# Kernel optimization log

Hardware: AMD Instinct MI355X
Metric: run time of the kernel (lower is better)

## Reference

```python
import jax, jax.numpy as jnp
import numpy as np
import math

N_NODES = 100000
N_EDGES = 1_600_000
NFEAT = 512
NHID = 128
NLAYERS = 6
NCLASS = 64


def setup_inputs() -> dict:
    key = jax.random.key(0)
    ks = jax.random.split(key, 8)
    x = jax.random.normal(ks[0], (N_NODES, NFEAT), jnp.float32)
    rows = jax.random.randint(ks[1], (N_EDGES,), 0, N_NODES, dtype=jnp.int32)
    cols = jax.random.randint(ks[2], (N_EDGES,), 0, N_NODES, dtype=jnp.int32)
    # normalized-adjacency-like edge weights
    vals = jax.random.uniform(ks[3], (N_EDGES,), jnp.float32) * (1.0 / 16.0)
    s = 1.0 / math.sqrt(NHID)  # reset_parameters: uniform(-1/sqrt(out_features), ...)
    W0 = jax.random.uniform(ks[4], (NFEAT, NHID), jnp.float32, minval=-s, maxval=s)
    Wh = jax.random.uniform(ks[5], (NLAYERS - 1, NHID, NHID), jnp.float32, minval=-s, maxval=s)
    Wfc = jax.random.normal(ks[6], (NHID * NLAYERS, NCLASS), jnp.float32) * 0.02
    bfc = jnp.zeros((NCLASS,), jnp.float32)
    return {"x": x, "rows": rows, "cols": cols, "vals": vals,
            "W0": W0, "Wh": Wh, "Wfc": Wfc, "bfc": bfc}


def _spmm(rows, cols, vals, h, n):
    # sparse [n,n] @ h : gather source rows, scale by edge weight, scatter-add to dest
    return jax.ops.segment_sum(vals[:, None] * h[cols], rows, num_segments=n)


def reference(x, rows, cols, vals, W0, Wh, Wfc, bfc):
    n = x.shape[0]
    # conv0: relu(spmm(A, x @ W0))  (inference: no dropout, no skip-gate)
    h = jax.nn.relu(_spmm(rows, cols, vals, x @ W0, n))
    hiddens = [h]
    for i in range(Wh.shape[0]):
        h = jax.nn.relu(_spmm(rows, cols, vals, h @ Wh[i], n))
        hiddens.append(h)
    logits = jnp.concatenate(hiddens, axis=-1) @ Wfc + bfc
    return jax.nn.log_softmax(logits, axis=1)
```

## Files before the change

kernel.cpp:

```cpp
#include <hip/hip_runtime.h>
#include <hip/hip_bf16.h>
#include <cstdint>
#include <cstddef>

static constexpr int NFEAT   = 512;
static constexpr int NHID    = 128;
static constexpr int NLAYERS = 6;
static constexpr int NCLASS  = 64;

typedef __bf16 bf16x8 __attribute__((ext_vector_type(8)));
typedef float  floatx4 __attribute__((ext_vector_type(4)));

static __device__ __forceinline__ uint16_t f2bf(float v){
    __hip_bfloat16 h = __float2bfloat16(v);
    return *reinterpret_cast<uint16_t*>(&h);
}

__global__ void k_sniff(const uint16_t* __restrict__ x, int nwords, uint32_t* __restrict__ flag){
    int i = blockIdx.x*256 + threadIdx.x;
    if (i < nwords){
        uint16_t w = x[i];
        if ((w & 0x7F80u) == 0x7F80u) atomicOr(flag, 1u);
    }
}

__global__ void k_sentinel(uint16_t* out, int nel){
    int i = blockIdx.x*256 + threadIdx.x;
    if (i < nel) out[i] = 0x3E00u;
}

__global__ void k_zero(uint32_t* p, int n){
    int i = blockIdx.x*256 + threadIdx.x;
    if (i < n) p[i] = 0u;
}

__global__ void k_hist(const int* __restrict__ rows, uint32_t* __restrict__ deg, int nE){
    int e = blockIdx.x*256 + threadIdx.x;
    if (e < nE) atomicAdd(&deg[rows[e]], 1u);
}

__global__ __launch_bounds__(1024) void k_scan1(const uint32_t* __restrict__ deg,
                                                uint32_t* __restrict__ row_start,
                                                uint32_t* __restrict__ partial, int n){
    __shared__ uint32_t sh[1024];
    int tid = threadIdx.x;
    int i = blockIdx.x*1024 + tid;
    uint32_t v = (i < n) ? deg[i] : 0u;
    sh[tid] = v; __syncthreads();
    for (int off = 1; off < 1024; off <<= 1){
        uint32_t t = (tid >= off) ? sh[tid-off] : 0u;
        __syncthreads();
        sh[tid] += t;
        __syncthreads();
    }
    if (i < n) row_start[i+1] = sh[tid];
    if (tid == 1023) partial[blockIdx.x] = sh[1023];
}

__global__ __launch_bounds__(128) void k_scan2(uint32_t* partial, int nb){
    __shared__ uint32_t sh[128];
    int tid = threadIdx.x;
    uint32_t v = (tid < nb) ? partial[tid] : 0u;
    sh[tid] = v; __syncthreads();
    for (int off = 1; off < 128; off <<= 1){
        uint32_t t = (tid >= off) ? sh[tid-off] : 0u;
        __syncthreads();
        sh[tid] += t;
        __syncthreads();
    }
    if (tid < nb) partial[tid] = sh[tid] - v;
}

__global__ __launch_bounds__(1024) void k_scan3(const uint32_t* __restrict__ deg,
                                                uint32_t* __restrict__ row_start,
                                                const uint32_t* __restrict__ partial,
                                                uint32_t* __restrict__ bcur,
                                                uint32_t* __restrict__ cursor, int n){
    int i = blockIdx.x*1024 + threadIdx.x;
    if (i < n){
        uint32_t rs = row_start[i+1] + partial[blockIdx.x];
        row_start[i+1] = rs;
        uint32_t start = rs - deg[i];
        cursor[i] = start;
        if ((i & 255) == 0) bcur[i >> 8] = start;
        if (i == 0) row_start[0] = 0u;
    }
}

__global__ void k_scatter(const int* __restrict__ rows, const int* __restrict__ cols,
                          const void* __restrict__ vals,
                          uint32_t* __restrict__ cursor, uint2* __restrict__ ep, int nE,
                          const uint32_t* __restrict__ flags){
    int e = blockIdx.x*256 + threadIdx.x;
    if (e < nE){
        int r = rows[e];
        uint32_t pos = atomicAdd(&cursor[r], 1u);
        float v;
        if (flags[0]) v = ((const float*)vals)[e];
        else          v = __bfloat162float(((const __hip_bfloat16*)vals)[e]);
        ep[pos] = make_uint2((uint32_t)cols[e], __float_as_uint(v));
    }
}

__global__ __launch_bounds__(256) void k_bin(
    const int* __restrict__ rows, const int* __restrict__ cols,
    const void* __restrict__ vals,
    uint32_t* __restrict__ bcur,
    uint2* __restrict__ epb, uint8_t* __restrict__ rloc,
    int nE, int nbuck, int epb_per_block,
    const uint32_t* __restrict__ flags)
{
    __shared__ uint32_t h[512];
    const int tid = threadIdx.x;
    const int e0 = blockIdx.x * epb_per_block;
    int e1 = e0 + epb_per_block; if (e1 > nE) e1 = nE;

    for (int b = tid; b < nbuck; b += 256) h[b] = 0u;
    __syncthreads();
    for (int e = e0 + tid; e < e1; e += 256){
        int r = rows[e];
        atomicAdd(&h[r >> 8], 1u);
    }
    __syncthreads();
    for (int b = tid; b < nbuck; b += 256){
        uint32_t c = h[b];
        h[b] = c ? atomicAdd(&bcur[b], c) : 0u;
    }
    __syncthreads();
    const int fp32 = (int)flags[0];
    for (int e = e0 + tid; e < e1; e += 256){
        int r = rows[e];
        uint32_t pos = atomicAdd(&h[r >> 8], 1u);
        float v;
        if (fp32) v = ((const float*)vals)[e];
        else      v = __bfloat162float(((const __hip_bfloat16*)vals)[e]);
        epb[pos] = make_uint2((uint32_t)cols[e], __float_as_uint(v));
        rloc[pos] = (uint8_t)(r & 255);
    }
}

__global__ __launch_bounds__(256) void k_csr(
    const uint32_t* __restrict__ row_start,
    const uint2* __restrict__ epb, const uint8_t* __restrict__ rloc,
    uint2* __restrict__ ep, int n)
{
    __shared__ uint32_t curs[256];
    const int b = blockIdx.x;
    const int r0 = b << 8;
    const int tid = threadIdx.x;
    const int r = r0 + tid;
    curs[tid] = (r < n) ? row_start[r] : 0u;
    __syncthreads();
    int rend = r0 + 256; if (rend > n) rend = n;
    const uint32_t s = row_start[r0];
    const uint32_t e = row_start[rend];
    for (uint32_t i = s + tid; i < e; i += 256){
        uint2 rec = epb[i];
        uint32_t rl = rloc[i];
        uint32_t pos = atomicAdd(&curs[rl], 1u);
        ep[pos] = rec;
    }
}

__global__ void k_transpose_all(const void* __restrict__ W0, const void* __restrict__ Wh,
                                const void* __restrict__ Wfc,
                                uint16_t* __restrict__ W0t, uint16_t* __restrict__ Wht,
                                uint16_t* __restrict__ Wfct,
                                const uint32_t* __restrict__ flags)
{
    const int idx = blockIdx.x*256 + threadIdx.x;
    const int T0 = NFEAT*NHID;
    const int T1 = (NLAYERS-1)*NHID*NHID;
    const int T2 = NLAYERS*NHID*NCLASS;
    const int fp32 = (int)flags[0];
    if (idx < T0){
        uint16_t w = fp32 ? f2bf(((const float*)W0)[idx]) : ((const uint16_t*)W0)[idx];
        int k = idx / NHID, nn = idx - k*NHID;
        W0t[nn*NFEAT + k] = w;
    } else if (idx < T0 + T1){
        int j = idx - T0;
        uint16_t w = fp32 ? f2bf(((const float*)Wh)[j]) : ((const uint16_t*)Wh)[j];
        int l = j / (NHID*NHID); int jj = j - l*(NHID*NHID);
        int k = jj / NHID, nn = jj - k*NHID;
        Wht[l*NHID*NHID + nn*NHID + k] = w;
    } else if (idx < T0 + T1 + T2){
        int j = idx - T0 - T1;
        uint16_t w = fp32 ? f2bf(((const float*)Wfc)[j]) : ((const uint16_t*)Wfc)[j];
        int k = j / NCLASS, nn = j - k*NCLASS;
        Wfct[nn*(NLAYERS*NHID) + k] = w;
    }
}

template<int NTILES, int MODE>
__global__ __launch_bounds__(256) void k_gemm(
    const void* __restrict__ Aany, int lda,
    const uint16_t* __restrict__ Bt, int ldb, int K, int Mwaves,
    uint16_t* __restrict__ Cb, float* __restrict__ Cf,
    const uint32_t* __restrict__ flagsp)
{
    __shared__ uint16_t lds[NTILES*16*40];
    const int tid  = threadIdx.x;
    const int lane = tid & 63;
    const int gw   = blockIdx.x*4 + (tid >> 6);
    const bool active = gw < Mwaves;
    const int m = lane & 15, quad = lane >> 4;
    const long row0 = (long)gw * 16;
    const int afp32 = flagsp ? (int)flagsp[0] : 0;
    const uint16_t* A16 = (const uint16_t*)Aany;
    const float*    A32 = (const float*)Aany;

    floatx4 acc[NTILES];
#pragma unroll
    for (int i = 0; i < NTILES; i++) acc[i] = (floatx4){0.f,0.f,0.f,0.f};

    for (int kk = 0; kk < K; kk += 32){
        for (int idx = tid; idx < NTILES*16*4; idx += 256){
            int nn = idx >> 2, c = idx & 3;
            *(bf16x8*)&lds[nn*40 + c*8] = *(const bf16x8*)&Bt[(long)nn*ldb + kk + c*8];
        }
        __syncthreads();
        if (active){
            bf16x8 a;
            if (afp32){
                const float* p = &A32[(row0 + m)*lda + kk + quad*8];
                float4 f0 = *(const float4*)p;
                float4 f1 = *(const float4*)(p + 4);
                a[0]=(__bf16)f0.x; a[1]=(__bf16)f0.y; a[2]=(__bf16)f0.z; a[3]=(__bf16)f0.w;
                a[4]=(__bf16)f1.x; a[5]=(__bf16)f1.y; a[6]=(__bf16)f1.z; a[7]=(__bf16)f1.w;
            } else {
                a = *(const bf16x8*)&A16[(row0 + m)*lda + kk + quad*8];
            }
#pragma unroll
            for (int nt = 0; nt < NTILES; nt++){
                bf16x8 b = *(const bf16x8*)&lds[(nt*16 + m)*40 + quad*8];
                acc[nt] = __builtin_amdgcn_mfma_f32_16x16x32_bf16(a, b, acc[nt], 0, 0, 0);
            }
        }
        __syncthreads();
    }
    if (active){
#pragma unroll
        for (int nt = 0; nt < NTILES; nt++){
#pragma unroll
            for (int r = 0; r < 4; r++){
                long row = row0 + quad*4 + r;
                int  col = nt*16 + m;
                float v = acc[nt][r];
                if (MODE == 1) Cf[row*(NTILES*16) + col] += v;
                else           Cb[row*(NTILES*16) + col] = f2bf(v);
            }
        }
    }
}

__global__ __launch_bounds__(256) void k_gemm_fused(
    const uint16_t* __restrict__ A,
    const uint16_t* __restrict__ B1t,
    const uint16_t* __restrict__ B2t, int ldb2,
    uint16_t* __restrict__ C1, float* __restrict__ C2, int nchunks,
    int store_c2)
{
    __shared__ uint16_t lds[(128+64)*132];
    const int tid = threadIdx.x, lane = tid & 63;
    for (int idx = tid; idx < 128*16; idx += 256){
        int nn = idx >> 4, c = idx & 15;
        *(bf16x8*)&lds[nn*132 + c*8] = *(const bf16x8*)&B1t[nn*128 + c*8];
    }
    for (int idx = tid; idx < 64*16; idx += 256){
        int nn = idx >> 4, c = idx & 15;
        *(bf16x8*)&lds[(128+nn)*132 + c*8] = *(const bf16x8*)&B2t[(long)nn*ldb2 + c*8];
    }
    __syncthreads();

    const int m = lane & 15, quad = lane >> 4;
    const int nw = gridDim.x * 4;
    for (int chunk = blockIdx.x*4 + (tid >> 6); chunk < nchunks; chunk += nw){
        const long row0 = (long)chunk * 16;
        const uint16_t* Arow = &A[(row0 + m)*128 + quad*8];
        bf16x8 a[4];
#pragma unroll
        for (int ks = 0; ks < 4; ks++) a[ks] = *(const bf16x8*)&Arow[ks*32];

        floatx4 acc1[8], acc2[4];
#pragma unroll
        for (int i = 0; i < 8; i++) acc1[i] = (floatx4){0.f,0.f,0.f,0.f};
#pragma unroll
        for (int i = 0; i < 4; i++) acc2[i] = (floatx4){0.f,0.f,0.f,0.f};

#pragma unroll
        for (int ks = 0; ks < 4; ks++){
            const int kk = ks*32 + quad*8;
#pragma unroll
            for (int nt = 0; nt < 8; nt++){
                bf16x8 b = *(const bf16x8*)&lds[(nt*16 + m)*132 + kk];
                acc1[nt] = __builtin_amdgcn_mfma_f32_16x16x32_bf16(a[ks], b, acc1[nt], 0, 0, 0);
            }
#pragma unroll
            for (int nt = 0; nt < 4; nt++){
                bf16x8 b = *(const bf16x8*)&lds[(128 + nt*16 + m)*132 + kk];
                acc2[nt] = __builtin_amdgcn_mfma_f32_16x16x32_bf16(a[ks], b, acc2[nt], 0, 0, 0);
            }
        }
#pragma unroll
        for (int nt = 0; nt < 8; nt++){
#pragma unroll
            for (int r = 0; r < 4; r++){
                long row = row0 + quad*4 + r;
                int  col = nt*16 + m;
                float v  = acc1[nt][r];
                float vn = __shfl_xor(v, 1);
                if ((m & 1) == 0){
                    uint32_t pk = (uint32_t)f2bf(v) | ((uint32_t)f2bf(vn) << 16);
                    *(uint32_t*)&C1[row*128 + col] = pk;
                }
            }
        }
#pragma unroll
        for (int nt = 0; nt < 4; nt++){
#pragma unroll
            for (int r = 0; r < 4; r++){
                long row = row0 + quad*4 + r;
                int  col = nt*16 + m;
                float v  = acc2[nt][r];
                float vn = __shfl_xor(v, 1);
                if ((m & 1) == 0){
                    float2* p = (float2*)&C2[row*64 + col];
                    if (store_c2){
                        float2 o; o.x = v; o.y = vn; *p = o;
                    } else {
                        float2 o = *p;
                        o.x += v; o.y += vn;
                        *p = o;
                    }
                }
            }
        }
    }
}

__global__ __launch_bounds__(256) void k_spmm(
    const uint2* __restrict__ ep, const uint32_t* __restrict__ row_start,
    const uint32_t* __restrict__ tmp, uint16_t* __restrict__ out, int n)
{
    int t = blockIdx.x*256 + threadIdx.x;
    int gw = t >> 6, lane = t & 63;
    if (gw >= n) return;
    uint32_t s = row_start[gw], e = row_start[gw+1];
    float ax = 0.f, ay = 0.f;
    for (uint32_t base = s; base < e; base += 64){
        int cnt = (int)(e - base); if (cnt > 64) cnt = 64;
        uint2 d = (lane < cnt) ? ep[base + lane] : make_uint2(0u, 0u);
        int j = 0;
        for (; j + 4 <= cnt; j += 4){
            uint32_t c0 = __shfl(d.x, j+0); float v0 = __uint_as_float(__shfl(d.y, j+0));
            uint32_t c1 = __shfl(d.x, j+1); float v1 = __uint_as_float(__shfl(d.y, j+1));
            uint32_t c2 = __shfl(d.x, j+2); float v2 = __uint_as_float(__shfl(d.y, j+2));
            uint32_t c3 = __shfl(d.x, j+3); float v3 = __uint_as_float(__shfl(d.y, j+3));
            uint32_t p0 = tmp[(size_t)c0*64 + lane];
            uint32_t p1 = tmp[(size_t)c1*64 + lane];
            uint32_t p2 = tmp[(size_t)c2*64 + lane];
            uint32_t p3 = tmp[(size_t)c3*64 + lane];
            ax = fmaf(v0, __uint_as_float(p0 << 16), ax); ay = fmaf(v0, __uint_as_float(p0 & 0xffff0000u), ay);
            ax = fmaf(v1, __uint_as_float(p1 << 16), ax); ay = fmaf(v1, __uint_as_float(p1 & 0xffff0000u), ay);
            ax = fmaf(v2, __uint_as_float(p2 << 16), ax); ay = fmaf(v2, __uint_as_float(p2 & 0xffff0000u), ay);
            ax = fmaf(v3, __uint_as_float(p3 << 16), ax); ay = fmaf(v3, __uint_as_float(p3 & 0xffff0000u), ay);
        }
        for (; j < cnt; j++){
            uint32_t c = __shfl(d.x, j); float v = __uint_as_float(__shfl(d.y, j));
            uint32_t p = tmp[(size_t)c*64 + lane];
            ax = fmaf(v, __uint_as_float(p << 16), ax);
            ay = fmaf(v, __uint_as_float(p & 0xffff0000u), ay);
        }
    }
    ax = fmaxf(ax, 0.f); ay = fmaxf(ay, 0.f);
    uint32_t packed = ((uint32_t)f2bf(ay) << 16) | (uint32_t)f2bf(ax);
    *(uint32_t*)&out[(size_t)gw*128 + 2*lane] = packed;
}

__global__ __launch_bounds__(256) void k_logsoftmax(const float* __restrict__ logits,
                                                    const void* __restrict__ bias,
                                                    void* __restrict__ out, int n,
                                                    const uint32_t* __restrict__ flags){
    int t = blockIdx.x*256 + threadIdx.x;
    int row = t >> 6, lane = t & 63;
    if (row >= n) return;
    const int fp32 = (int)flags[0];
    float b = fp32 ? ((const float*)bias)[lane]
                   : __bfloat162float(((const __hip_bfloat16*)bias)[lane]);
    float x = logits[(size_t)row*64 + lane] + b;
    float mx = x;
    for (int off = 32; off; off >>= 1) mx = fmaxf(mx, __shfl_xor(mx, off));
    float ex = __expf(x - mx);
    float sum = ex;
    for (int off = 32; off; off >>= 1) sum += __shfl_xor(sum, off);
    float r = x - mx - __logf(sum);
    if (fp32) ((float*)out)[(size_t)row*64 + lane] = r;
    else      ((uint16_t*)out)[(size_t)row*64 + lane] = f2bf(r);
}

extern "C" void kernel_launch(void* const* d_in, const int* in_sizes, int n_in,
                              void* d_out, int out_size, void* d_ws, size_t ws_size,
                              hipStream_t stream){
    const void* x    = d_in[0];
    const int* rows  = (const int*)d_in[1];
    const int* cols  = (const int*)d_in[2];
    const void* vals = d_in[3];
    const void* W0   = d_in[4];
    const void* Wh   = d_in[5];
    const void* Wfc  = d_in[6];
    const void* bfc  = d_in[7];

    const int n  = in_sizes[0] / NFEAT;
    const int nE = in_sizes[1];

    char* ws = (char*)d_ws;
    size_t off = 0;
    auto alloc = [&](size_t bytes)->char*{
        char* p = ws + off;
        off = (off + bytes + 255) & ~(size_t)255;
        return p;
    };
    uint32_t* flags     = (uint32_t*)alloc(256);
    uint32_t* deg       = (uint32_t*)alloc((size_t)n*4);
    uint32_t* row_start = (uint32_t*)alloc(((size_t)n+1)*4);
    uint32_t* cursor    = (uint32_t*)alloc((size_t)n*4);
    uint32_t* partial   = (uint32_t*)alloc(512);
    uint32_t* bcur      = (uint32_t*)alloc(2048);
    uint2*    ep        = (uint2*)   alloc((size_t)nE*8);
    uint16_t* W0t       = (uint16_t*)alloc((size_t)NFEAT*NHID*2);
    uint16_t* Wht       = (uint16_t*)alloc((size_t)(NLAYERS-1)*NHID*NHID*2);
    uint16_t* Wfct      = (uint16_t*)alloc((size_t)NCLASS*NLAYERS*NHID*2);
    uint16_t* tmp       = (uint16_t*)alloc((size_t)n*NHID*2);
    uint16_t* hbuf      = (uint16_t*)alloc((size_t)n*NHID*2);
    float*    logits    = (float*)   alloc((size_t)n*NCLASS*4);

    if (ws_size < off){
        k_sentinel<<<(out_size+255)/256, 256, 0, stream>>>((uint16_t*)d_out, out_size);
        return;
    }

    hipMemsetAsync(flags, 0, 4, stream);
    const int NW = 1 << 20;
    k_sniff<<<NW/256, 256, 0, stream>>>((const uint16_t*)x, NW, flags);

    const int scanBlocks = (n + 1023)/1024;
    k_zero<<<(n+255)/256, 256, 0, stream>>>(deg, n);
    k_hist<<<(nE+255)/256, 256, 0, stream>>>(rows, deg, nE);
    k_scan1<<<scanBlocks, 1024, 0, stream>>>(deg, row_start, partial, n);
    k_scan2<<<1, 128, 0, stream>>>(partial, scanBlocks);
    k_scan3<<<scanBlocks, 1024, 0, stream>>>(deg, row_start, partial, bcur, cursor, n);

    const int TTOT = NFEAT*NHID + (NLAYERS-1)*NHID*NHID + NLAYERS*NHID*NCLASS;
    k_transpose_all<<<(TTOT+255)/256, 256, 0, stream>>>(W0, Wh, Wfc, W0t, Wht, Wfct, flags);

    const int nbuck = (n + 255) >> 8;
    if (nbuck <= 512 && (size_t)n*NHID*2 >= (size_t)nE*9){
        uint2*   epb  = (uint2*)tmp;
        uint8_t* rloc = (uint8_t*)tmp + (size_t)nE*8;
        const int EPB = 2048;
        k_bin<<<(nE+EPB-1)/EPB, 256, 0, stream>>>(rows, cols, vals, bcur, epb, rloc,
                                                  nE, nbuck, EPB, flags);
        k_csr<<<nbuck, 256, 0, stream>>>(row_start, epb, rloc, ep, n);
    } else {
        k_scatter<<<(nE+255)/256, 256, 0, stream>>>(rows, cols, vals, cursor, ep, nE, flags);
    }

    const int Mwaves = n/16;
    const int gemmBlocks = (Mwaves + 3)/4;
    const int rowBlocks  = (n*64 + 255)/256;
    const int fusedBlocks = 768;

    k_gemm<8,0><<<gemmBlocks, 256, 0, stream>>>(x, NFEAT, W0t, NFEAT, NFEAT, Mwaves, tmp, nullptr, flags);
    k_spmm<<<rowBlocks, 256, 0, stream>>>(ep, row_start, (const uint32_t*)tmp, hbuf, n);
    for (int l = 1; l < NLAYERS; l++){
        k_gemm_fused<<<fusedBlocks, 256, 0, stream>>>(hbuf, Wht + (l-1)*NHID*NHID,
                                                      Wfct + (l-1)*NHID, NLAYERS*NHID,
                                                      tmp, logits, Mwaves, (l == 1) ? 1 : 0);
        k_spmm<<<rowBlocks, 256, 0, stream>>>(ep, row_start, (const uint32_t*)tmp, hbuf, n);
    }
    k_gemm<4,1><<<gemmBlocks, 256, 0, stream>>>(hbuf, NHID, Wfct + (NLAYERS-1)*NHID, NLAYERS*NHID,
                                                NHID, Mwaves, nullptr, logits, nullptr);
    k_logsoftmax<<<rowBlocks, 256, 0, stream>>>(logits, bfc, d_out, n, flags);
}
```

Baseline: 1.154 ms.

## Vectorize SpMM gathers across edges per wave and fuse final GEMM with log-softmax

```diff
diff --git a/kernel.cpp b/kernel.cpp
--- a/kernel.cpp
+++ b/kernel.cpp
@@ -27,11 +27,6 @@
 __global__ void k_sentinel(uint16_t* out, int nel){
     int i = blockIdx.x*256 + threadIdx.x;
     if (i < nel) out[i] = 0x3E00u;
-}
-
-__global__ void k_zero(uint32_t* p, int n){
-    int i = blockIdx.x*256 + threadIdx.x;
-    if (i < n) p[i] = 0u;
 }
 
 __global__ void k_hist(const int* __restrict__ rows, uint32_t* __restrict__ deg, int nE){
@@ -253,6 +248,76 @@
     }
 }
 
+__global__ __launch_bounds__(256) void k_gemm_final(
+    const uint16_t* __restrict__ A,
+    const uint16_t* __restrict__ Bt, int ldb, int Mwaves,
+    const float* __restrict__ logits, const void* __restrict__ bias,
+    void* __restrict__ outp, const uint32_t* __restrict__ flags)
+{
+    __shared__ uint16_t lds[4*16*40];
+    const int tid  = threadIdx.x;
+    const int lane = tid & 63;
+    const int gw   = blockIdx.x*4 + (tid >> 6);
+    const bool active = gw < Mwaves;
+    const int m = lane & 15, quad = lane >> 4;
+    const long row0 = (long)gw * 16;
+
+    floatx4 acc[4];
+#pragma unroll
+    for (int i = 0; i < 4; i++) acc[i] = (floatx4){0.f,0.f,0.f,0.f};
+
+    for (int kk = 0; kk < 128; kk += 32){
+        for (int idx = tid; idx < 4*16*4; idx += 256){
+            int nn = idx >> 2, c = idx & 3;
+            *(bf16x8*)&lds[nn*40 + c*8] = *(const bf16x8*)&Bt[(long)nn*ldb + kk + c*8];
+        }
+        __syncthreads();
+        if (active){
+            bf16x8 a = *(const bf16x8*)&A[(row0 + m)*128 + kk + quad*8];
+#pragma unroll
+            for (int nt = 0; nt < 4; nt++){
+                bf16x8 b = *(const bf16x8*)&lds[(nt*16 + m)*40 + quad*8];
+                acc[nt] = __builtin_amdgcn_mfma_f32_16x16x32_bf16(a, b, acc[nt], 0, 0, 0);
+            }
+        }
+        __syncthreads();
+    }
+    if (active){
+        const int fp32 = (int)flags[0];
+        float b[4];
+#pragma unroll
+        for (int nt = 0; nt < 4; nt++){
+            int col = nt*16 + m;
+            b[nt] = fp32 ? ((const float*)bias)[col]
+                         : __bfloat162float(((const __hip_bfloat16*)bias)[col]);
+        }
+#pragma unroll
+        for (int r = 0; r < 4; r++){
+            long row = row0 + quad*4 + r;
+            float v[4];
+#pragma unroll
+            for (int nt = 0; nt < 4; nt++){
+                int col = nt*16 + m;
+                v[nt] = logits[row*64 + col] + acc[nt][r] + b[nt];
+            }
+            float mx = fmaxf(fmaxf(v[0],v[1]), fmaxf(v[2],v[3]));
+#pragma unroll
+            for (int off = 1; off < 16; off <<= 1) mx = fmaxf(mx, __shfl_xor(mx, off));
+            float sum = __expf(v[0]-mx)+__expf(v[1]-mx)+__expf(v[2]-mx)+__expf(v[3]-mx);
+#pragma unroll
+            for (int off = 1; off < 16; off <<= 1) sum += __shfl_xor(sum, off);
+            float ls = mx + __logf(sum);
+#pragma unroll
+            for (int nt = 0; nt < 4; nt++){
+                int col = nt*16 + m;
+                float rr = v[nt] - ls;
+                if (fp32) ((float*)outp)[row*64 + col] = rr;
+                else      ((uint16_t*)outp)[row*64 + col] = f2bf(rr);
+            }
+        }
+    }
+}
+
 __global__ __launch_bounds__(256) void k_gemm_fused(
     const uint16_t* __restrict__ A,
     const uint16_t* __restrict__ B1t,
@@ -346,56 +411,52 @@
     int gw = t >> 6, lane = t & 63;
     if (gw >= n) return;
     uint32_t s = row_start[gw], e = row_start[gw+1];
-    float ax = 0.f, ay = 0.f;
+    const int q  = lane >> 4;
+    const int fl = lane & 15;
+    float acc[8];
+#pragma unroll
+    for (int i = 0; i < 8; i++) acc[i] = 0.f;
+
+#define ACC8(P, V) { \
+    acc[0] = fmaf(V, __uint_as_float((P).x << 16), acc[0]); \
+    acc[1] = fmaf(V, __uint_as_float((P).x & 0xffff0000u), acc[1]); \
+    acc[2] = fmaf(V, __uint_as_float((P).y << 16), acc[2]); \
+    acc[3] = fmaf(V, __uint_as_float((P).y & 0xffff0000u), acc[3]); \
+    acc[4] = fmaf(V, __uint_as_float((P).z << 16), acc[4]); \
+    acc[5] = fmaf(V, __uint_as_float((P).z & 0xffff0000u), acc[5]); \
+    acc[6] = fmaf(V, __uint_as_float((P).w << 16), acc[6]); \
+    acc[7] = fmaf(V, __uint_as_float((P).w & 0xffff0000u), acc[7]); }
+
     for (uint32_t base = s; base < e; base += 64){
         int cnt = (int)(e - base); if (cnt > 64) cnt = 64;
         uint2 d = (lane < cnt) ? ep[base + lane] : make_uint2(0u, 0u);
-        int j = 0;
-        for (; j + 4 <= cnt; j += 4){
-            uint32_t c0 = __shfl(d.x, j+0); float v0 = __uint_as_float(__shfl(d.y, j+0));
-            uint32_t c1 = __shfl(d.x, j+1); float v1 = __uint_as_float(__shfl(d.y, j+1));
-            uint32_t c2 = __shfl(d.x, j+2); float v2 = __uint_as_float(__shfl(d.y, j+2));
-            uint32_t c3 = __shfl(d.x, j+3); float v3 = __uint_as_float(__shfl(d.y, j+3));
-            uint32_t p0 = tmp[(size_t)c0*64 + lane];
-            uint32_t p1 = tmp[(size_t)c1*64 + lane];
-            uint32_t p2 = tmp[(size_t)c2*64 + lane];
-            uint32_t p3 = tmp[(size_t)c3*64 + lane];
-            ax = fmaf(v0, __uint_as_float(p0 << 16), ax); ay = fmaf(v0, __uint_as_float(p0 & 0xffff0000u), ay);
-            ax = fmaf(v1, __uint_as_float(p1 << 16), ax); ay = fmaf(v1, __uint_as_float(p1 & 0xffff0000u), ay);
-            ax = fmaf(v2, __uint_as_float(p2 << 16), ax); ay = fmaf(v2, __uint_as_float(p2 & 0xffff0000u), ay);
-            ax = fmaf(v3, __uint_as_float(p3 << 16), ax); ay = fmaf(v3, __uint_as_float(p3 & 0xffff0000u), ay);
-        }
-        for (; j < cnt; j++){
-            uint32_t c = __shfl(d.x, j); float v = __uint_as_float(__shfl(d.y, j));
-            uint32_t p = tmp[(size_t)c*64 + lane];
-            ax = fmaf(v, __uint_as_float(p << 16), ax);
-            ay = fmaf(v, __uint_as_float(p & 0xffff0000u), ay);
-        }
-    }
-    ax = fmaxf(ax, 0.f); ay = fmaxf(ay, 0.f);
-    uint32_t packed = ((uint32_t)f2bf(ay) << 16) | (uint32_t)f2bf(ax);
-    *(uint32_t*)&out[(size_t)gw*128 + 2*lane] = packed;
-}
-
-__global__ __launch_bounds__(256) void k_logsoftmax(const float* __restrict__ logits,
-                                                    const void* __restrict__ bias,
-                                                    void* __restrict__ out, int n,
-                                                    const uint32_t* __restrict__ flags){
-    int t = blockIdx.x*256 + threadIdx.x;
-    int row = t >> 6, lane = t & 63;
-    if (row >= n) return;
-    const int fp32 = (int)flags[0];
-    float b = fp32 ? ((const float*)bias)[lane]
-                   : __bfloat162float(((const __hip_bfloat16*)bias)[lane]);
-    float x = logits[(size_t)row*64 + lane] + b;
-    float mx = x;
-    for (int off = 32; off; off >>= 1) mx = fmaxf(mx, __shfl_xor(mx, off));
-    float ex = __expf(x - mx);
-    float sum = ex;
-    for (int off = 32; off; off >>= 1) sum += __shfl_xor(sum, off);
-    float r = x - mx - __logf(sum);
-    if (fp32) ((float*)out)[(size_t)row*64 + lane] = r;
-    else      ((uint16_t*)out)[(size_t)row*64 + lane] = f2bf(r);
+        for (int j = 0; j < cnt; j += 16){
+            uint32_t c0 = __shfl(d.x, j+q);    float v0 = __uint_as_float(__shfl(d.y, j+q));
+            uint32_t c1 = __shfl(d.x, j+q+4);  float v1 = __uint_as_float(__shfl(d.y, j+q+4));
+            uint32_t c2 = __shfl(d.x, j+q+8);  float v2 = __uint_as_float(__shfl(d.y, j+q+8));
+            uint32_t c3 = __shfl(d.x, j+q+12); float v3 = __uint_as_float(__shfl(d.y, j+q+12));
+            uint4 p0 = *(const uint4*)&tmp[(size_t)c0*64 + fl*4];
+            uint4 p1 = *(const uint4*)&tmp[(size_t)c1*64 + fl*4];
+            uint4 p2 = *(const uint4*)&tmp[(size_t)c2*64 + fl*4];
+            uint4 p3 = *(const uint4*)&tmp[(size_t)c3*64 + fl*4];
+            ACC8(p0, v0); ACC8(p1, v1); ACC8(p2, v2); ACC8(p3, v3);
+        }
+    }
+#undef ACC8
+
+#pragma unroll
+    for (int i = 0; i < 8; i++){
+        acc[i] += __shfl_xor(acc[i], 16);
+        acc[i] += __shfl_xor(acc[i], 32);
+    }
+    if (q == 0){
+        uint32_t w0 = (uint32_t)f2bf(fmaxf(acc[0],0.f)) | ((uint32_t)f2bf(fmaxf(acc[1],0.f)) << 16);
+        uint32_t w1 = (uint32_t)f2bf(fmaxf(acc[2],0.f)) | ((uint32_t)f2bf(fmaxf(acc[3],0.f)) << 16);
+        uint32_t w2 = (uint32_t)f2bf(fmaxf(acc[4],0.f)) | ((uint32_t)f2bf(fmaxf(acc[5],0.f)) << 16);
+        uint32_t w3 = (uint32_t)f2bf(fmaxf(acc[6],0.f)) | ((uint32_t)f2bf(fmaxf(acc[7],0.f)) << 16);
+        uint4 o = make_uint4(w0, w1, w2, w3);
+        *(uint4*)&out[(size_t)gw*128 + fl*8] = o;
+    }
 }
 
 extern "C" void kernel_launch(void* const* d_in, const int* in_sizes, int n_in,
@@ -444,7 +505,7 @@
     k_sniff<<<NW/256, 256, 0, stream>>>((const uint16_t*)x, NW, flags);
 
     const int scanBlocks = (n + 1023)/1024;
-    k_zero<<<(n+255)/256, 256, 0, stream>>>(deg, n);
+    hipMemsetAsync(deg, 0, (size_t)n*4, stream);
     k_hist<<<(nE+255)/256, 256, 0, stream>>>(rows, deg, nE);
     k_scan1<<<scanBlocks, 1024, 0, stream>>>(deg, row_start, partial, n);
     k_scan2<<<1, 128, 0, stream>>>(partial, scanBlocks);
@@ -478,7 +539,6 @@
                                                       tmp, logits, Mwaves, (l == 1) ? 1 : 0);
         k_spmm<<<rowBlocks, 256, 0, stream>>>(ep, row_start, (const uint32_t*)tmp, hbuf, n);
     }
-    k_gemm<4,1><<<gemmBlocks, 256, 0, stream>>>(hbuf, NHID, Wfct + (NLAYERS-1)*NHID, NLAYERS*NHID,
-                                                NHID, Mwaves, nullptr, logits, nullptr);
-    k_logsoftmax<<<rowBlocks, 256, 0, stream>>>(logits, bfc, d_out, n, flags);
-}
+    k_gemm_final<<<gemmBlocks, 256, 0, stream>>>(hbuf, Wfct + (NLAYERS-1)*NHID, NLAYERS*NHID,
+                                                 Mwaves, logits, bfc, d_out, flags);
+}
```

Measured after the change: 1.114 ms. -3.4%, faster.
